# Performance work log

Hardware: AMD Instinct MI355X
Metric: run time of the kernel (lower is better)

## Reference

```python
import jax, jax.numpy as jnp
import numpy as np

D, H, O, NEXP, NA = 128, 256, 128, 8, 5  # na = max(1, int(8*0.7)) = 5
T = float(np.e)  # gate temperature
N_TOKENS = 131072


def ternary_quantize(w):
    # per-expert-matrix threshold: alpha = mean(|W|) over each [out,in] matrix
    alpha = jnp.mean(jnp.abs(w), axis=(-2, -1), keepdims=True)
    return jnp.sign(w) * (jnp.abs(w) > 0.5 * alpha).astype(w.dtype)


def setup_inputs() -> dict:
    key = jax.random.key(0)
    ks = jax.random.split(key, 7)
    x = jax.random.normal(ks[0], (N_TOKENS, D), dtype=jnp.float32)
    # expert params stacked over expert dim e (nn.Linear layout: [out, in])
    w1 = jax.random.normal(ks[1], (NEXP, H, D), dtype=jnp.float32) * 0.05
    b1 = jax.random.normal(ks[2], (NEXP, H), dtype=jnp.float32) * 0.05
    w2 = jax.random.normal(ks[3], (NEXP, O, H), dtype=jnp.float32) * 0.05
    b2 = jax.random.normal(ks[4], (NEXP, O), dtype=jnp.float32) * 0.05
    wg = jax.random.normal(ks[5], (NEXP, D), dtype=jnp.float32) * 0.05
    bg = jax.random.normal(ks[6], (NEXP,), dtype=jnp.float32) * 0.05
    return {"x": x, "w1": w1, "b1": b1, "w2": w2, "b2": b2, "wg": wg, "bg": bg}


def reference(x, w1, b1, w2, b2, wg, bg):
    # Ternary-quantize expert weights on the fly (TW.forward); dropout in eval mode (identity).
    w1q = ternary_quantize(w1)
    w2q = ternary_quantize(w2)
    # all-expert dense MLP: x [t,d] -> hidden [t,e,h] -> eo [t,e,o]
    hid = jax.nn.relu(jnp.einsum('td,ehd->teh', x, w1q) + b1[None, :, :])
    eo = jnp.einsum('teh,eoh->teo', hid, w2q) + b2[None, :, :]
    # BG gate: tempered softmax, top-k mask, renormalize
    p = jax.nn.softmax((x @ wg.T + bg) / T, axis=-1)          # [t,e]
    _, idx = jax.lax.top_k(p, NA)                             # [t,na]
    m = jnp.sum(jax.nn.one_hot(idx, NEXP, dtype=p.dtype), axis=-2)  # [t,e] 0/1 mask
    w = p * m
    w = w / (jnp.sum(w, axis=-1, keepdims=True) + 1e-8)
    return jnp.einsum('te,teo->to', w, eo)
```

## Files before the change

kernel.cpp:

```cpp
#include <hip/hip_runtime.h>
#include <hip/hip_bf16.h>

typedef unsigned int u32;
typedef unsigned char u8;
typedef unsigned short u16;
using f32x4  = __attribute__((ext_vector_type(4))) float;
using f32x16 = __attribute__((ext_vector_type(16))) float;
using u32x4  = __attribute__((ext_vector_type(4))) u32;
using s16x8  = __attribute__((ext_vector_type(8))) short;

#define DEV static __device__ __forceinline__

DEV u32 pk2(float a, float b) {
  u16 lo = __builtin_bit_cast(u16, __float2bfloat16(a));
  u16 hi = __builtin_bit_cast(u16, __float2bfloat16(b));
  return (u32)lo | ((u32)hi << 16);
}

DEV f32x16 MFMA32(u32x4 a, u32x4 b, f32x16 c) {
  return __builtin_amdgcn_mfma_f32_32x32x16_bf16(
      __builtin_bit_cast(s16x8, a), __builtin_bit_cast(s16x8, b), c, 0, 0, 0);
}

DEV void pl32swap(u32& a, u32& b) {
  asm volatile("v_permlane32_swap_b32 %0, %1" : "+v"(a), "+v"(b));
}

typedef const __attribute__((address_space(1))) u32 gu32;
typedef __attribute__((address_space(3))) u32 lu32;

DEV void load_lds16(const void* g, void* l) {
  __builtin_amdgcn_global_load_lds((gu32*)g, (lu32*)l, 16, 0, 0);
}

DEV u16 tq1(float v, float thr) {
  return (fabsf(v) > thr) ? (v > 0.f ? (u16)0x3F80 : (u16)0xBF80) : (u16)0;
}
DEV u32 tq2(float a, float b, float thr) {
  return (u32)tq1(a, thr) | ((u32)tq1(b, thr) << 16);
}

__global__ void k_img_gate(const float* __restrict__ w1,
                           const float* __restrict__ w2,
                           char* __restrict__ img, const float* __restrict__ x,
                           const float* __restrict__ wg,
                           const float* __restrict__ bg, float* __restrict__ gw,
                           u8* __restrict__ maskA, u32* __restrict__ hist) {
  const int tid = threadIdx.x;
  if (blockIdx.x < 256) {
    const int b = blockIdx.x;
    const float* wsrc = (b < 128) ? (w1 + (size_t)(b >> 4) * 32768)
                                  : (w2 + (size_t)((b - 128) >> 4) * 32768);
    float s = 0.f;
    const float4* wv4 = (const float4*)wsrc;
    #pragma unroll
    for (int j = 0; j < 32; ++j) {
      float4 v = wv4[tid + j * 256];
      s += fabsf(v.x) + fabsf(v.y) + fabsf(v.z) + fabsf(v.w);
    }
    #pragma unroll
    for (int off = 32; off >= 1; off >>= 1) s += __shfl_down(s, off, 64);
    __shared__ float ws4[4];
    if ((tid & 63) == 0) ws4[tid >> 6] = s;
    __syncthreads();
    const float thr =
        0.5f * (ws4[0] + ws4[1] + ws4[2] + ws4[3]) * (1.f / 32768.f);

    int gid = b * 256 + tid;
    int l = gid & 63;
    int col = l & 31, hi = l >> 5;
    const float* src;
    char* dst;
    if (gid < 32768) {
      int ks = (gid >> 6) & 7;
      int n  = gid >> 9;
      int e  = n >> 3, ht = n & 7;
      int h  = ht * 32 + col;
      int k0 = ks * 16 + hi * 8;
      src = w1 + (size_t)e * 32768 + h * 128 + k0;
      dst = img + (size_t)n * 16384 + ks * 1024 + l * 16;
    } else {
      int id = gid - 32768;
      int sl = (id >> 6) & 7;
      int n  = id >> 9;
      int e  = n >> 3, c = n & 7;
      int ks2 = sl >> 2, ot = sl & 3;
      int o  = ot * 32 + col;
      int k0 = c * 32 + ks2 * 16 + hi * 8;
      src = w2 + (size_t)e * 32768 + o * 256 + k0;
      dst = img + (size_t)n * 16384 + 8192 + sl * 1024 + l * 16;
    }
    float4 v0 = *(const float4*)src;
    float4 v1 = *(const float4*)(src + 4);
    *(uint4*)dst = make_uint4(tq2(v0.x, v0.y, thr), tq2(v0.z, v0.w, thr),
                              tq2(v1.x, v1.y, thr), tq2(v1.z, v1.w, thr));
    return;
  }
  __shared__ float s_wg[1024];
  __shared__ float s_bg[8];
  __shared__ u32 lh[256];
  ((float4*)s_wg)[tid] = ((const float4*)wg)[tid];
  if (tid < 8) s_bg[tid] = bg[tid];
  lh[tid] = 0;
  __syncthreads();

  int t = (blockIdx.x - 256) * 256 + tid;
  const float4* xr = (const float4*)(x + (size_t)t * 128);
  float lg[8];
  #pragma unroll
  for (int e = 0; e < 8; ++e) lg[e] = s_bg[e];
  for (int i = 0; i < 32; ++i) {
    float4 xv = xr[i];
    #pragma unroll
    for (int e = 0; e < 8; ++e) {
      f32x4 wv = *(const f32x4*)(s_wg + e * 128 + i * 4);
      lg[e] += xv.x * wv.x + xv.y * wv.y + xv.z * wv.z + xv.w * wv.w;
    }
  }
  const float invT = 0.36787944117144233f;
  #pragma unroll
  for (int e = 0; e < 8; ++e) lg[e] *= invT;
  float mx = lg[0];
  #pragma unroll
  for (int e = 1; e < 8; ++e) mx = fmaxf(mx, lg[e]);
  float p[8], den = 0.f;
  #pragma unroll
  for (int e = 0; e < 8; ++e) { p[e] = __expf(lg[e] - mx); den += p[e]; }
  float inv = 1.f / den;
  #pragma unroll
  for (int e = 0; e < 8; ++e) p[e] *= inv;
  float gsel[8], wsum = 0.f;
  u32 m = 0;
  #pragma unroll
  for (int e = 0; e < 8; ++e) {
    int rank = 0;
    #pragma unroll
    for (int e2 = 0; e2 < 8; ++e2)
      rank += (p[e2] > p[e]) || (p[e2] == p[e] && e2 < e);
    bool sel = rank < 5;
    if (sel) m |= 1u << e;
    gsel[e] = sel ? p[e] : 0.f;
    wsum += gsel[e];
  }
  float r = 1.f / (wsum + 1e-8f);
  float* gwp = gw + (size_t)t * 8;
  *(f32x4*)gwp       = (f32x4){gsel[0] * r, gsel[1] * r, gsel[2] * r, gsel[3] * r};
  *(f32x4*)(gwp + 4) = (f32x4){gsel[4] * r, gsel[5] * r, gsel[6] * r, gsel[7] * r};
  maskA[t] = (u8)m;
  __syncthreads();
  atomicAdd(&lh[m], 1u);
  __syncthreads();
  if (lh[tid]) atomicAdd(&hist[tid << 5], lh[tid]);
}

__global__ void k_scatter(const u32* __restrict__ hist, const u8* __restrict__ maskA,
                          u32* __restrict__ cur2, u32* __restrict__ perm,
                          u32* __restrict__ order, u32* __restrict__ umask) {
  const int t = threadIdx.x;
  if (blockIdx.x < 512) {
    __shared__ u32 s[256], lh[256], lb[256];
    u32 h = hist[t << 5];
    s[t] = h;
    lh[t] = 0;
    __syncthreads();
    #pragma unroll
    for (int o = 1; o < 256; o <<= 1) {
      u32 v = (t >= o) ? s[t - o] : 0u;
      __syncthreads();
      s[t] += v;
      __syncthreads();
    }
    const u32 pbase = s[t] - h;
    int tkn = blockIdx.x * 256 + t;
    u32 m = maskA[tkn];
    u32 r = atomicAdd(&lh[m], 1u);
    __syncthreads();
    if (lh[t]) lb[t] = pbase + atomicAdd(&cur2[t << 5], lh[t]);
    __syncthreads();
    perm[lb[m] + r] = (u32)tkn;
    return;
  }
  __shared__ u32 sh[256], sA[256], spfx[256];
  __shared__ u32 bcnt[4], bcur[4], boff[4];
  __shared__ u32 L[512];
  u32 h = hist[t << 5];
  sh[t] = h;
  sA[t] = h;
  if (t < 4) { bcnt[t] = 0; bcur[t] = 0; }
  __syncthreads();
  #pragma unroll
  for (int o = 1; o < 256; o <<= 1) {
    u32 v = (t >= o) ? sA[t - o] : 0u;
    __syncthreads();
    sA[t] += v;
    __syncthreads();
  }
  spfx[t] = sA[t] - h;
  __syncthreads();
  int c[2];
  int mb[2] = {t, t + 256};
  #pragma unroll
  for (int k = 0; k < 2; ++k) {
    u32 start = (u32)mb[k] * 256u, end = start + 256u;
    u32 un = 0;
    for (int m = 0; m < 256; ++m) {
      u32 p0 = spfx[m];
      if (sh[m] && p0 < end && p0 + sh[m] > start) un |= (u32)m;
    }
    umask[mb[k]] = un;
    c[k] = (int)__popc(un);
    atomicAdd(&bcnt[8 - c[k]], 1);
  }
  __syncthreads();
  if (t == 0) {
    boff[0] = 0;
    boff[1] = bcnt[0];
    boff[2] = bcnt[0] + bcnt[1];
    boff[3] = bcnt[0] + bcnt[1] + bcnt[2];
  }
  __syncthreads();
  #pragma unroll
  for (int k = 0; k < 2; ++k) {
    int q = 8 - c[k];
    u32 pos = boff[q] + atomicAdd(&bcur[q], 1);
    L[pos] = (u32)mb[k];
  }
  __syncthreads();
  order[2 * t]     = L[t];
  order[2 * t + 1] = L[511 - t];
}

#define B1_OFF 65536
#define G_OFF  73728
#define SMEM_BYTES 81920

__global__ __launch_bounds__(256, 2) void moe_main(
    const float* __restrict__ x, const float* __restrict__ b1g,
    const float* __restrict__ b2g, const char* __restrict__ img,
    const u32* __restrict__ perm, const float* __restrict__ gw,
    const u32* __restrict__ order, const u32* __restrict__ umask,
    float* __restrict__ out) {
  extern __shared__ char smem[];
  float* s_b1 = (float*)(smem + B1_OFF);
  float* s_g  = (float*)(smem + G_OFF);
  const int tid = threadIdx.x;
  const int w = tid >> 6, l = tid & 63;
  const int col = l & 31, hi = l >> 5;
  const int bid = (int)order[blockIdx.x];
  const int base = bid * 256;
  const u32 loff = (u32)(l * 16);

  const u32 bmask = __builtin_amdgcn_readfirstlane(umask[bid]);
  u32 elist = 0;
  int cnt = 0;
  #pragma unroll
  for (int e = 0; e < 8; ++e)
    if ((bmask >> e) & 1) { elist |= (u32)e << (4 * cnt); ++cnt; }
  elist = __builtin_amdgcn_readfirstlane(elist);
  const int iters = __builtin_amdgcn_readfirstlane(cnt * 4);

  auto stage_pair = [&](int P, int slot) {
    const char* src = img + (size_t)P * 32768 + w * 8192 + loff;
    char* dst = smem + slot * 32768 + w * 8192;
    #pragma unroll
    for (int i = 0; i < 8; ++i)
      load_lds16(src + i * 1024, dst + i * 1024);
  };

  stage_pair((elist & 7) * 4, 0);

  u32x4 xf[2][8];
  {
    const u32 ptg = perm[base + tid];
    f32x4 gA = *(const f32x4*)(gw + (size_t)ptg * 8);
    f32x4 gB = *(const f32x4*)(gw + (size_t)ptg * 8 + 4);
    s_g[0 * 256 + tid] = gA.x; s_g[1 * 256 + tid] = gA.y;
    s_g[2 * 256 + tid] = gA.z; s_g[3 * 256 + tid] = gA.w;
    s_g[4 * 256 + tid] = gB.x; s_g[5 * 256 + tid] = gB.y;
    s_g[6 * 256 + tid] = gB.z; s_g[7 * 256 + tid] = gB.w;
    const float4* s = (const float4*)b1g;
    float4* d = (float4*)s_b1;
    d[tid] = s[tid];
    d[tid + 256] = s[tid + 256];

    #pragma unroll
    for (int tt = 0; tt < 2; ++tt) {
      const u32 pt = perm[base + w * 64 + tt * 32 + col];
      #pragma unroll
      for (int ks = 0; ks < 8; ++ks) {
        const float* xp = x + (size_t)pt * 128 + ks * 16 + hi * 8;
        float4 v0 = *(const float4*)xp;
        float4 v1 = *(const float4*)(xp + 4);
        xf[tt][ks] = (u32x4){pk2(v0.x, v0.y), pk2(v0.z, v0.w),
                             pk2(v1.x, v1.y), pk2(v1.z, v1.w)};
      }
    }
  }
  __syncthreads();

  f32x16 acc2[4][2];
  {
    u32x4 gf[2];
    #pragma unroll
    for (int tt = 0; tt < 2; ++tt) {
      u32x4 v = (u32x4){0u, 0u, 0u, 0u};
      if (hi == 0) {
        int t = w * 64 + tt * 32 + col;
        v = (u32x4){pk2(s_g[0 * 256 + t], s_g[1 * 256 + t]),
                    pk2(s_g[2 * 256 + t], s_g[3 * 256 + t]),
                    pk2(s_g[4 * 256 + t], s_g[5 * 256 + t]),
                    pk2(s_g[6 * 256 + t], s_g[7 * 256 + t])};
      }
      gf[tt] = v;
    }
    #pragma unroll
    for (int ot = 0; ot < 4; ++ot) {
      u32x4 af = (u32x4){0u, 0u, 0u, 0u};
      if (hi == 0) {
        int o = ot * 32 + col;
        af = (u32x4){pk2(b2g[0 * 128 + o], b2g[1 * 128 + o]),
                     pk2(b2g[2 * 128 + o], b2g[3 * 128 + o]),
                     pk2(b2g[4 * 128 + o], b2g[5 * 128 + o]),
                     pk2(b2g[6 * 128 + o], b2g[7 * 128 + o])};
      }
      f32x16 z{};
      #pragma unroll
      for (int tt = 0; tt < 2; ++tt) acc2[ot][tt] = MFMA32(af, gf[tt], z);
    }
  }

  auto chunk = [&](const char* cb, int e, int ht, float g0, float g1) {
    f32x16 a1_0{}, a1_1{};
    __builtin_amdgcn_s_setprio(1);
    #pragma unroll
    for (int ks = 0; ks < 8; ++ks) {
      u32x4 f = *(const u32x4*)(cb + ks * 1024 + loff);
      a1_0 = MFMA32(f, xf[0][ks], a1_0);
      a1_1 = MFMA32(f, xf[1][ks], a1_1);
    }
    __builtin_amdgcn_s_setprio(0);

    const float* b1b = s_b1 + e * 256 + ht * 32 + hi * 4;
    u32x4 hf[2][2];
    #pragma unroll
    for (int tt = 0; tt < 2; ++tt) {
      const f32x16& a1 = tt ? a1_1 : a1_0;
      const float g = tt ? g1 : g0;
      u32 u[8];
      #pragma unroll
      for (int rg = 0; rg < 4; ++rg) {
        f32x4 bb = *(const f32x4*)(b1b + rg * 8);
        float h0 = fmaxf(a1[rg * 4 + 0] + bb.x, 0.f) * g;
        float h1 = fmaxf(a1[rg * 4 + 1] + bb.y, 0.f) * g;
        float h2 = fmaxf(a1[rg * 4 + 2] + bb.z, 0.f) * g;
        float h3 = fmaxf(a1[rg * 4 + 3] + bb.w, 0.f) * g;
        u[rg * 2 + 0] = pk2(h0, h1);
        u[rg * 2 + 1] = pk2(h2, h3);
      }
      pl32swap(u[0], u[2]);
      pl32swap(u[1], u[3]);
      pl32swap(u[4], u[6]);
      pl32swap(u[5], u[7]);
      hf[0][tt] = (u32x4){u[0], u[1], u[2], u[3]};
      hf[1][tt] = (u32x4){u[4], u[5], u[6], u[7]};
    }

    __builtin_amdgcn_s_setprio(1);
    #pragma unroll
    for (int ks2 = 0; ks2 < 2; ++ks2) {
      #pragma unroll
      for (int ot = 0; ot < 4; ++ot) {
        u32x4 af = *(const u32x4*)(cb + 8192 + (ks2 * 4 + ot) * 1024 + loff);
        acc2[ot][0] = MFMA32(af, hf[ks2][0], acc2[ot][0]);
        acc2[ot][1] = MFMA32(af, hf[ks2][1], acc2[ot][1]);
      }
    }
    __builtin_amdgcn_s_setprio(0);
  };

  #pragma unroll 1
  for (int i = 0; i < iters; ++i) {
    asm volatile("s_waitcnt vmcnt(0)" ::: "memory");
    __builtin_amdgcn_s_barrier();
    __builtin_amdgcn_sched_barrier(0);
    if (i + 1 < iters) {
      const int j = i + 1;
      const int ej = (elist >> (4 * (j >> 2))) & 7;
      stage_pair(ej * 4 + (j & 3), j & 1);
    }
    const int ei = (elist >> (4 * (i >> 2))) & 7;
    const int ht0 = (i & 3) * 2;
    const float g0 = s_g[ei * 256 + w * 64 + col];
    const float g1 = s_g[ei * 256 + w * 64 + 32 + col];
    const char* buf = smem + (i & 1) * 32768;
    chunk(buf, ei, ht0, g0, g1);
    __builtin_amdgcn_sched_barrier(0);
    chunk(buf + 16384, ei, ht0 + 1, g0, g1);
  }

  #pragma unroll
  for (int tt = 0; tt < 2; ++tt) {
    const u32 pt = perm[base + w * 64 + tt * 32 + col];
    #pragma unroll
    for (int ot = 0; ot < 4; ++ot) {
      const f32x16& a = acc2[ot][tt];
      float* op = out + (size_t)pt * 128 + ot * 32 + hi * 4;
      #pragma unroll
      for (int rg = 0; rg < 4; ++rg)
        *(f32x4*)(op + rg * 8) =
            (f32x4){a[rg * 4 + 0], a[rg * 4 + 1], a[rg * 4 + 2], a[rg * 4 + 3]};
    }
  }
}

extern "C" void kernel_launch(void* const* d_in, const int* in_sizes, int n_in,
                              void* d_out, int out_size, void* d_ws, size_t ws_size,
                              hipStream_t stream) {
  const float* x  = (const float*)d_in[0];
  const float* w1 = (const float*)d_in[1];
  const float* b1 = (const float*)d_in[2];
  const float* w2 = (const float*)d_in[3];
  const float* b2 = (const float*)d_in[4];
  const float* wg = (const float*)d_in[5];
  const float* bg = (const float*)d_in[6];
  float* out = (float*)d_out;

  int ntok = in_sizes[0] / 128;
  int nblk = ntok / 256;

  char* ws = (char*)d_ws;
  char*  img    = ws;
  u32*   hist   = (u32*)(ws + 1048576);
  u32*   cur2   = (u32*)(ws + 1081344);
  u32*   order  = (u32*)(ws + 1114112);
  u32*   umask  = (u32*)(ws + 1116160);
  u8*    maskA  = (u8*)(ws + 1118208);
  u32*   perm   = (u32*)(ws + 1249280);
  float* gw     = (float*)(ws + 1773568);
  if (ws_size < 5967872) return;

  hipMemsetAsync(hist, 0, 65536, stream);
  k_img_gate<<<256 + nblk, 256, 0, stream>>>(w1, w2, img, x, wg, bg,
                                             gw, maskA, hist);
  k_scatter<<<nblk + 1, 256, 0, stream>>>(hist, maskA, cur2, perm, order, umask);

  hipFuncSetAttribute(reinterpret_cast<const void*>(moe_main),
                      hipFuncAttributeMaxDynamicSharedMemorySize, SMEM_BYTES);
  moe_main<<<nblk, 256, SMEM_BYTES, stream>>>(x, b1, b2, img, perm, gw,
                                              order, umask, out);
}
```

Measured before the change: 162.3 us.

## Fuse gate and scatter kernels with a grid-wide spin barrier

Merges the gating/histogram kernel and the scatter/order kernel into one launch. Gate blocks publish their histogram, then spin on a global done counter until every gate block has arrived, and only then compute the prefix scan and scatter their own tokens into perm. This drops a kernel launch, the maskA round trip and the re-read of the mask, but it relies on all 512 gate blocks being co-resident. If they are not, the grid can deadlock, and spinning blocks can also delay the weight-image blocks.

Measured after the change: 256.6 us. 58.2% more time.

```diff
diff --git a/kernel.cpp b/kernel.cpp
--- a/kernel.cpp
+++ b/kernel.cpp
@@ -40,12 +40,13 @@
   return (u32)tq1(a, thr) | ((u32)tq1(b, thr) << 16);
 }
 
-__global__ void k_img_gate(const float* __restrict__ w1,
-                           const float* __restrict__ w2,
-                           char* __restrict__ img, const float* __restrict__ x,
-                           const float* __restrict__ wg,
-                           const float* __restrict__ bg, float* __restrict__ gw,
-                           u8* __restrict__ maskA, u32* __restrict__ hist) {
+__global__ void k_fused(const float* __restrict__ w1, const float* __restrict__ w2,
+                        char* __restrict__ img, const float* __restrict__ x,
+                        const float* __restrict__ wg, const float* __restrict__ bg,
+                        float* __restrict__ gw, u32* __restrict__ hist,
+                        u32* __restrict__ cur2, u32* __restrict__ perm,
+                        u32* __restrict__ order, u32* __restrict__ umask,
+                        u32* __restrict__ done, int ngate) {
   const int tid = threadIdx.x;
   if (blockIdx.x < 256) {
     const int b = blockIdx.x;
@@ -96,15 +97,19 @@
                               tq2(v1.x, v1.y, thr), tq2(v1.z, v1.w, thr));
     return;
   }
+
   __shared__ float s_wg[1024];
   __shared__ float s_bg[8];
-  __shared__ u32 lh[256];
+  __shared__ u32 lh[256], s_scan[256], sh2[256], spfx[256], lb[256];
+  __shared__ u32 bcnt[4], bcur[4], boff[4];
+  __shared__ u32 L[512];
+
   ((float4*)s_wg)[tid] = ((const float4*)wg)[tid];
   if (tid < 8) s_bg[tid] = bg[tid];
   lh[tid] = 0;
   __syncthreads();
 
-  int t = (blockIdx.x - 256) * 256 + tid;
+  const int t = (blockIdx.x - 256) * 256 + tid;
   const float4* xr = (const float4*)(x + (size_t)t * 128);
   float lg[8];
   #pragma unroll
@@ -146,88 +151,73 @@
   float* gwp = gw + (size_t)t * 8;
   *(f32x4*)gwp       = (f32x4){gsel[0] * r, gsel[1] * r, gsel[2] * r, gsel[3] * r};
   *(f32x4*)(gwp + 4) = (f32x4){gsel[4] * r, gsel[5] * r, gsel[6] * r, gsel[7] * r};
-  maskA[t] = (u8)m;
-  __syncthreads();
-  atomicAdd(&lh[m], 1u);
+  __syncthreads();
+  const u32 myrank = atomicAdd(&lh[m], 1u);
   __syncthreads();
   if (lh[tid]) atomicAdd(&hist[tid << 5], lh[tid]);
-}
-
-__global__ void k_scatter(const u32* __restrict__ hist, const u8* __restrict__ maskA,
-                          u32* __restrict__ cur2, u32* __restrict__ perm,
-                          u32* __restrict__ order, u32* __restrict__ umask) {
-  const int t = threadIdx.x;
-  if (blockIdx.x < 512) {
-    __shared__ u32 s[256], lh[256], lb[256];
-    u32 h = hist[t << 5];
-    s[t] = h;
-    lh[t] = 0;
-    __syncthreads();
-    #pragma unroll
-    for (int o = 1; o < 256; o <<= 1) {
-      u32 v = (t >= o) ? s[t - o] : 0u;
-      __syncthreads();
-      s[t] += v;
-      __syncthreads();
-    }
-    const u32 pbase = s[t] - h;
-    int tkn = blockIdx.x * 256 + t;
-    u32 m = maskA[tkn];
-    u32 r = atomicAdd(&lh[m], 1u);
-    __syncthreads();
-    if (lh[t]) lb[t] = pbase + atomicAdd(&cur2[t << 5], lh[t]);
-    __syncthreads();
-    perm[lb[m] + r] = (u32)tkn;
-    return;
-  }
-  __shared__ u32 sh[256], sA[256], spfx[256];
-  __shared__ u32 bcnt[4], bcur[4], boff[4];
-  __shared__ u32 L[512];
-  u32 h = hist[t << 5];
-  sh[t] = h;
-  sA[t] = h;
-  if (t < 4) { bcnt[t] = 0; bcur[t] = 0; }
+  __threadfence();
+  __syncthreads();
+  if (tid == 0) {
+    atomicAdd(done, 1u);
+    while (__hip_atomic_load(done, __ATOMIC_ACQUIRE,
+                             __HIP_MEMORY_SCOPE_AGENT) < (u32)ngate)
+      __builtin_amdgcn_s_sleep(2);
+  }
+  __syncthreads();
+
+  const u32 h = __hip_atomic_load(&hist[tid << 5], __ATOMIC_RELAXED,
+                                  __HIP_MEMORY_SCOPE_AGENT);
+  s_scan[tid] = h;
+  sh2[tid] = h;
   __syncthreads();
   #pragma unroll
   for (int o = 1; o < 256; o <<= 1) {
-    u32 v = (t >= o) ? sA[t - o] : 0u;
-    __syncthreads();
-    sA[t] += v;
-    __syncthreads();
-  }
-  spfx[t] = sA[t] - h;
-  __syncthreads();
-  int c[2];
-  int mb[2] = {t, t + 256};
-  #pragma unroll
-  for (int k = 0; k < 2; ++k) {
-    u32 start = (u32)mb[k] * 256u, end = start + 256u;
-    u32 un = 0;
-    for (int m = 0; m < 256; ++m) {
-      u32 p0 = spfx[m];
-      if (sh[m] && p0 < end && p0 + sh[m] > start) un |= (u32)m;
-    }
-    umask[mb[k]] = un;
-    c[k] = (int)__popc(un);
-    atomicAdd(&bcnt[8 - c[k]], 1);
-  }
-  __syncthreads();
-  if (t == 0) {
-    boff[0] = 0;
-    boff[1] = bcnt[0];
-    boff[2] = bcnt[0] + bcnt[1];
-    boff[3] = bcnt[0] + bcnt[1] + bcnt[2];
-  }
-  __syncthreads();
-  #pragma unroll
-  for (int k = 0; k < 2; ++k) {
-    int q = 8 - c[k];
-    u32 pos = boff[q] + atomicAdd(&bcur[q], 1);
-    L[pos] = (u32)mb[k];
-  }
-  __syncthreads();
-  order[2 * t]     = L[t];
-  order[2 * t + 1] = L[511 - t];
+    u32 v = (tid >= o) ? s_scan[tid - o] : 0u;
+    __syncthreads();
+    s_scan[tid] += v;
+    __syncthreads();
+  }
+  const u32 pb = s_scan[tid] - h;
+  spfx[tid] = pb;
+  if (lh[tid]) lb[tid] = pb + atomicAdd(&cur2[tid << 5], lh[tid]);
+  __syncthreads();
+  perm[lb[m] + myrank] = (u32)t;
+
+  if (blockIdx.x == 256) {
+    if (tid < 4) { bcnt[tid] = 0; bcur[tid] = 0; }
+    __syncthreads();
+    int c[2];
+    int mb[2] = {tid, tid + 256};
+    #pragma unroll
+    for (int k = 0; k < 2; ++k) {
+      u32 start = (u32)mb[k] * 256u, end = start + 256u;
+      u32 un = 0;
+      for (int bm = 0; bm < 256; ++bm) {
+        u32 p0 = spfx[bm];
+        if (sh2[bm] && p0 < end && p0 + sh2[bm] > start) un |= (u32)bm;
+      }
+      umask[mb[k]] = un;
+      c[k] = (int)__popc(un);
+      atomicAdd(&bcnt[8 - c[k]], 1);
+    }
+    __syncthreads();
+    if (tid == 0) {
+      boff[0] = 0;
+      boff[1] = bcnt[0];
+      boff[2] = bcnt[0] + bcnt[1];
+      boff[3] = bcnt[0] + bcnt[1] + bcnt[2];
+    }
+    __syncthreads();
+    #pragma unroll
+    for (int k = 0; k < 2; ++k) {
+      int q = 8 - c[k];
+      u32 pos = boff[q] + atomicAdd(&bcur[q], 1);
+      L[pos] = (u32)mb[k];
+    }
+    __syncthreads();
+    order[2 * tid]     = L[tid];
+    order[2 * tid + 1] = L[511 - tid];
+  }
 }
 
 #define B1_OFF 65536
@@ -432,17 +422,16 @@
   char*  img    = ws;
   u32*   hist   = (u32*)(ws + 1048576);
   u32*   cur2   = (u32*)(ws + 1081344);
-  u32*   order  = (u32*)(ws + 1114112);
-  u32*   umask  = (u32*)(ws + 1116160);
-  u8*    maskA  = (u8*)(ws + 1118208);
-  u32*   perm   = (u32*)(ws + 1249280);
-  float* gw     = (float*)(ws + 1773568);
-  if (ws_size < 5967872) return;
-
-  hipMemsetAsync(hist, 0, 65536, stream);
-  k_img_gate<<<256 + nblk, 256, 0, stream>>>(w1, w2, img, x, wg, bg,
-                                             gw, maskA, hist);
-  k_scatter<<<nblk + 1, 256, 0, stream>>>(hist, maskA, cur2, perm, order, umask);
+  u32*   done   = (u32*)(ws + 1114112);
+  u32*   order  = (u32*)(ws + 1114176);
+  u32*   umask  = (u32*)(ws + 1116224);
+  u32*   perm   = (u32*)(ws + 1118272);
+  float* gw     = (float*)(ws + 1642560);
+  if (ws_size < 5836864) return;
+
+  hipMemsetAsync(hist, 0, 65600, stream);
+  k_fused<<<256 + nblk, 256, 0, stream>>>(w1, w2, img, x, wg, bg, gw, hist,
+                                          cur2, perm, order, umask, done, nblk);
 
   hipFuncSetAttribute(reinterpret_cast<const void*>(moe_main),
                       hipFuncAttributeMaxDynamicSharedMemorySize, SMEM_BYTES);
```

## Move weight ternarization into scatter kernel and split gate into its own kernel

Applied to the files above, without the earlier changes.

The weight-image ternarization blocks move out of the gate kernel and are fused with the scatter kernel, and the gate kernel is now standalone with a fully unrolled dot-product loop. The idea is to rebalance the two pre-processing launches so the weight quantization overlaps with the scatter work rather than with the heavy gate pass. The scatter grid is hardcoded to 768+1 blocks, which assumes nblk equals 512 and breaks for any other token count.

After: 162.1 us. Within noise of the previous version (-0.1%).

```diff
diff --git a/kernel.cpp b/kernel.cpp
--- a/kernel.cpp
+++ b/kernel.cpp
@@ -40,12 +40,79 @@
   return (u32)tq1(a, thr) | ((u32)tq1(b, thr) << 16);
 }
 
-__global__ void k_img_gate(const float* __restrict__ w1,
-                           const float* __restrict__ w2,
-                           char* __restrict__ img, const float* __restrict__ x,
-                           const float* __restrict__ wg,
-                           const float* __restrict__ bg, float* __restrict__ gw,
-                           u8* __restrict__ maskA, u32* __restrict__ hist) {
+__global__ void k_gate(const float* __restrict__ x, const float* __restrict__ wg,
+                       const float* __restrict__ bg, float* __restrict__ gw,
+                       u8* __restrict__ maskA, u32* __restrict__ hist) {
+  const int tid = threadIdx.x;
+  __shared__ float s_wg[1024];
+  __shared__ float s_bg[8];
+  __shared__ u32 lh[256];
+  ((float4*)s_wg)[tid] = ((const float4*)wg)[tid];
+  if (tid < 8) s_bg[tid] = bg[tid];
+  lh[tid] = 0;
+  __syncthreads();
+
+  int t = blockIdx.x * 256 + tid;
+  const float4* xr = (const float4*)(x + (size_t)t * 128);
+  float lg[8];
+  #pragma unroll
+  for (int e = 0; e < 8; ++e) lg[e] = s_bg[e];
+  #pragma unroll
+  for (int c = 0; c < 4; ++c) {
+    #pragma unroll
+    for (int ii = 0; ii < 8; ++ii) {
+      int i = c * 8 + ii;
+      float4 xv = xr[i];
+      #pragma unroll
+      for (int e = 0; e < 8; ++e) {
+        f32x4 wv = *(const f32x4*)(s_wg + e * 128 + i * 4);
+        lg[e] += xv.x * wv.x + xv.y * wv.y + xv.z * wv.z + xv.w * wv.w;
+      }
+    }
+  }
+  const float invT = 0.36787944117144233f;
+  #pragma unroll
+  for (int e = 0; e < 8; ++e) lg[e] *= invT;
+  float mx = lg[0];
+  #pragma unroll
+  for (int e = 1; e < 8; ++e) mx = fmaxf(mx, lg[e]);
+  float p[8], den = 0.f;
+  #pragma unroll
+  for (int e = 0; e < 8; ++e) { p[e] = __expf(lg[e] - mx); den += p[e]; }
+  float inv = 1.f / den;
+  #pragma unroll
+  for (int e = 0; e < 8; ++e) p[e] *= inv;
+  float gsel[8], wsum = 0.f;
+  u32 m = 0;
+  #pragma unroll
+  for (int e = 0; e < 8; ++e) {
+    int rank = 0;
+    #pragma unroll
+    for (int e2 = 0; e2 < 8; ++e2)
+      rank += (p[e2] > p[e]) || (p[e2] == p[e] && e2 < e);
+    bool sel = rank < 5;
+    if (sel) m |= 1u << e;
+    gsel[e] = sel ? p[e] : 0.f;
+    wsum += gsel[e];
+  }
+  float r = 1.f / (wsum + 1e-8f);
+  float* gwp = gw + (size_t)t * 8;
+  *(f32x4*)gwp       = (f32x4){gsel[0] * r, gsel[1] * r, gsel[2] * r, gsel[3] * r};
+  *(f32x4*)(gwp + 4) = (f32x4){gsel[4] * r, gsel[5] * r, gsel[6] * r, gsel[7] * r};
+  maskA[t] = (u8)m;
+  __syncthreads();
+  atomicAdd(&lh[m], 1u);
+  __syncthreads();
+  if (lh[tid]) atomicAdd(&hist[tid << 5], lh[tid]);
+}
+
+__global__ void k_img_scatter(const float* __restrict__ w1,
+                              const float* __restrict__ w2,
+                              char* __restrict__ img,
+                              const u32* __restrict__ hist,
+                              const u8* __restrict__ maskA,
+                              u32* __restrict__ cur2, u32* __restrict__ perm,
+                              u32* __restrict__ order, u32* __restrict__ umask) {
   const int tid = threadIdx.x;
   if (blockIdx.x < 256) {
     const int b = blockIdx.x;
@@ -96,69 +163,9 @@
                               tq2(v1.x, v1.y, thr), tq2(v1.z, v1.w, thr));
     return;
   }
-  __shared__ float s_wg[1024];
-  __shared__ float s_bg[8];
-  __shared__ u32 lh[256];
-  ((float4*)s_wg)[tid] = ((const float4*)wg)[tid];
-  if (tid < 8) s_bg[tid] = bg[tid];
-  lh[tid] = 0;
-  __syncthreads();
-
-  int t = (blockIdx.x - 256) * 256 + tid;
-  const float4* xr = (const float4*)(x + (size_t)t * 128);
-  float lg[8];
-  #pragma unroll
-  for (int e = 0; e < 8; ++e) lg[e] = s_bg[e];
-  for (int i = 0; i < 32; ++i) {
-    float4 xv = xr[i];
-    #pragma unroll
-    for (int e = 0; e < 8; ++e) {
-      f32x4 wv = *(const f32x4*)(s_wg + e * 128 + i * 4);
-      lg[e] += xv.x * wv.x + xv.y * wv.y + xv.z * wv.z + xv.w * wv.w;
-    }
-  }
-  const float invT = 0.36787944117144233f;
-  #pragma unroll
-  for (int e = 0; e < 8; ++e) lg[e] *= invT;
-  float mx = lg[0];
-  #pragma unroll
-  for (int e = 1; e < 8; ++e) mx = fmaxf(mx, lg[e]);
-  float p[8], den = 0.f;
-  #pragma unroll
-  for (int e = 0; e < 8; ++e) { p[e] = __expf(lg[e] - mx); den += p[e]; }
-  float inv = 1.f / den;
-  #pragma unroll
-  for (int e = 0; e < 8; ++e) p[e] *= inv;
-  float gsel[8], wsum = 0.f;
-  u32 m = 0;
-  #pragma unroll
-  for (int e = 0; e < 8; ++e) {
-    int rank = 0;
-    #pragma unroll
-    for (int e2 = 0; e2 < 8; ++e2)
-      rank += (p[e2] > p[e]) || (p[e2] == p[e] && e2 < e);
-    bool sel = rank < 5;
-    if (sel) m |= 1u << e;
-    gsel[e] = sel ? p[e] : 0.f;
-    wsum += gsel[e];
-  }
-  float r = 1.f / (wsum + 1e-8f);
-  float* gwp = gw + (size_t)t * 8;
-  *(f32x4*)gwp       = (f32x4){gsel[0] * r, gsel[1] * r, gsel[2] * r, gsel[3] * r};
-  *(f32x4*)(gwp + 4) = (f32x4){gsel[4] * r, gsel[5] * r, gsel[6] * r, gsel[7] * r};
-  maskA[t] = (u8)m;
-  __syncthreads();
-  atomicAdd(&lh[m], 1u);
-  __syncthreads();
-  if (lh[tid]) atomicAdd(&hist[tid << 5], lh[tid]);
-}
-
-__global__ void k_scatter(const u32* __restrict__ hist, const u8* __restrict__ maskA,
-                          u32* __restrict__ cur2, u32* __restrict__ perm,
-                          u32* __restrict__ order, u32* __restrict__ umask) {
-  const int t = threadIdx.x;
-  if (blockIdx.x < 512) {
+  if (blockIdx.x < 768) {
     __shared__ u32 s[256], lh[256], lb[256];
+    const int t = tid;
     u32 h = hist[t << 5];
     s[t] = h;
     lh[t] = 0;
@@ -171,7 +178,7 @@
       __syncthreads();
     }
     const u32 pbase = s[t] - h;
-    int tkn = blockIdx.x * 256 + t;
+    int tkn = (blockIdx.x - 256) * 256 + t;
     u32 m = maskA[tkn];
     u32 r = atomicAdd(&lh[m], 1u);
     __syncthreads();
@@ -183,6 +190,7 @@
   __shared__ u32 sh[256], sA[256], spfx[256];
   __shared__ u32 bcnt[4], bcur[4], boff[4];
   __shared__ u32 L[512];
+  const int t = tid;
   u32 h = hist[t << 5];
   sh[t] = h;
   sA[t] = h;
@@ -440,9 +448,9 @@
   if (ws_size < 5967872) return;
 
   hipMemsetAsync(hist, 0, 65536, stream);
-  k_img_gate<<<256 + nblk, 256, 0, stream>>>(w1, w2, img, x, wg, bg,
-                                             gw, maskA, hist);
-  k_scatter<<<nblk + 1, 256, 0, stream>>>(hist, maskA, cur2, perm, order, umask);
+  k_gate<<<nblk, 256, 0, stream>>>(x, wg, bg, gw, maskA, hist);
+  k_img_scatter<<<768 + 1, 256, 0, stream>>>(w1, w2, img, hist, maskA,
+                                             cur2, perm, order, umask);
 
   hipFuncSetAttribute(reinterpret_cast<const void*>(moe_main),
                       hipFuncAttributeMaxDynamicSharedMemorySize, SMEM_BYTES);
```
